# Kernel tuning notes

Measured on AMD Instinct MI355X. Metric: run time of the kernel, lower is better.

## Reference

```python
import jax, jax.numpy as jnp
import numpy as np
from jax.scipy.special import logsumexp

B, N, F_IN, HID = 8, 1024, 256, 128
RATIO = 0.5
NUM_LAYERS = 2
EPS_OT = 0.01  # forward default epsilon


def setup_inputs():
    key = jax.random.key(0)
    ks = jax.random.split(key, 6)
    x = jax.random.normal(ks[0], (B, N, F_IN), dtype=jnp.float32)
    adj = (jax.random.uniform(ks[1], (B, N, N)) < 0.02).astype(jnp.float32)
    adj = jnp.maximum(adj, jnp.swapaxes(adj, 1, 2))  # symmetric sparse-ish graph
    mask = jnp.ones((B, N), dtype=bool)
    W1 = jax.random.normal(ks[2], (F_IN, HID), dtype=jnp.float32) / np.sqrt(F_IN)
    b1 = jnp.zeros((HID,), dtype=jnp.float32)
    Watt = jax.random.normal(ks[3], (HID, 1), dtype=jnp.float32) / np.sqrt(HID)
    batt = jnp.zeros((1,), dtype=jnp.float32)
    W2 = jax.random.normal(ks[4], (HID, F_IN), dtype=jnp.float32) / np.sqrt(HID)
    b2 = jnp.zeros((F_IN,), dtype=jnp.float32)
    return dict(x=x, adj=adj, mask=mask, W1=W1, b1=b1, Watt=Watt, batt=batt,
                W2=W2, b2=b2, opt_epochs=20)


def _gcn_norm(adj):
    # DenseGCNConv add_loop + symmetric normalization
    n = adj.shape[-1]
    A = adj + jnp.eye(n, dtype=adj.dtype)
    d = jnp.maximum(A.sum(-1), 1.0) ** -0.5
    return d[..., :, None] * A * d[..., None, :]


def dense_gcn(x, adj, W, b, mask=None):
    out = jnp.einsum('bij,bjh->bih', _gcn_norm(adj), x @ W) + b
    if mask is not None:
        out = out * mask[..., None].astype(out.dtype)
    return out


def normalize_batch_adj(adj):
    # CoarsenBlock.normalize_batch_adj: self-loop sym-norm, zero-row masked
    n = adj.shape[-1]
    A = adj + jnp.eye(n, dtype=adj.dtype)
    d = jnp.maximum(A.sum(-1), 1.0) ** -0.5
    newA = d[..., :, None] * A * d[..., None, :]
    return (adj.sum(-1) > 0).astype(adj.dtype)[..., None] * newA


def coarsen_block(x, adj, Watt, batt):
    # attention score per node, squared then sigmoid  -> [B, N]
    alpha = jax.nn.sigmoid(dense_gcn(x, adj, Watt, batt) ** 2)[..., 0]
    norm_adj = normalize_batch_adj(adj)
    k = int(adj.shape[1] * RATIO) + 1
    cut = jax.lax.top_k(alpha, k)[0][:, -1]                 # per-sample k-th value
    cut_alpha = jax.nn.relu(alpha + 1e-7 - cut[:, None])    # soft top-k gate
    S = norm_adj * cut_alpha[:, None, :]
    S = S / jnp.maximum(jnp.abs(S).sum(-1, keepdims=True), 1e-12)  # row L1 norm
    emb = jnp.einsum('bij,bif->bjf', S, x)                  # S^T x
    tmp = jnp.einsum('bij,bik->bjk', S, adj)                # S^T adj
    new_adj = jnp.einsum('bjk,bkl->bjl', tmp, S)            # S^T adj S
    return emb, new_adj, S


def sinkhorn_loss(x, y, eps, niter):
    # squared-euclidean cost via gram trick (no [n,m,f] intermediate)
    C = (jnp.sum(x * x, -1)[:, None] + jnp.sum(y * y, -1)[None, :]
         - 2.0 * (x @ y.T))
    n, m = C.shape
    log_mu = jnp.full((n,), -np.log(n), dtype=C.dtype)
    log_nu = jnp.full((m,), -np.log(m), dtype=C.dtype)

    def M(u, v):
        return (-C + u[:, None] + v[None, :]) / eps

    def step(carry, _):
        u, v = carry
        u = eps * (log_mu - logsumexp(M(u, v), axis=1)) + u
        v = eps * (log_nu - logsumexp(M(u, v), axis=0)) + v
        return (u, v), None

    (u, v), _ = jax.lax.scan(step, (jnp.zeros_like(log_mu), jnp.zeros_like(log_nu)),
                             None, length=niter)
    pi = jnp.exp(M(u, v))
    return jnp.sum(pi * C)


def reference(x, adj, mask, W1, b1, Watt, batt, W2, b2, opt_epochs):
    x1 = jax.nn.relu(dense_gcn(x, adj, W1, b1, mask))
    xs0 = x1.mean(axis=1)
    new_adjs = [adj]
    Ss = []
    coarse_x, new_adj = x1, adj
    for _ in range(NUM_LAYERS):
        coarse_x, new_adj, S = coarsen_block(coarse_x, new_adj, Watt, batt)
        new_adjs.append(new_adj)
        Ss.append(S)
    x2 = dense_gcn(coarse_x, new_adj, W2, b2, mask)
    xs1 = x2.mean(axis=1)
    loss_fn = lambda a, b: sinkhorn_loss(a, b, EPS_OT, opt_epochs)
    opt_loss = jnp.sum(jax.vmap(loss_fn)(x, x2))
    return (xs0, xs1, new_adjs[0], new_adjs[1], new_adjs[2], Ss[0], Ss[1], opt_loss)
```

## Files before the change

### kernel.cpp

```cpp
#include <hip/hip_runtime.h>
#include <math.h>

#define BN   8
#define NN   1024
#define FIN  256
#define HIDN 128
#define KTOP 513
#define NITER 20
#define EPS_S 0.01f
#define INV_EPS 100.0f
#define LOG_MU (-6.9314718055994531f)
#define SNB 256

typedef __attribute__((ext_vector_type(8))) short bfrag8;
typedef __attribute__((ext_vector_type(4))) float facc4;

#define GLOAD16(g, l) __builtin_amdgcn_global_load_lds( \
    (const __attribute__((address_space(1))) unsigned int*)(g), \
    (__attribute__((address_space(3))) unsigned int*)(l), 16, 0, 0)

static __device__ __forceinline__ float wred_sum(float s) {
#pragma unroll
  for (int o = 32; o > 0; o >>= 1) s += __shfl_xor(s, o);
  return s;
}
static __device__ __forceinline__ unsigned short f2b(float f) {
  unsigned int u = __float_as_uint(f);
  u += 0x7fff + ((u >> 16) & 1);
  return (unsigned short)(u >> 16);
}
static __device__ __forceinline__ float b2f(unsigned short h) {
  return __uint_as_float((unsigned int)h << 16);
}

template<int WRBF, int WCOPY>
__global__ __launch_bounds__(256) void k_rowstats4(const float* __restrict__ adj,
                                                   float* __restrict__ dv,
                                                   float* __restrict__ rm,
                                                   unsigned short* __restrict__ abf,
                                                   float* __restrict__ ocopy) {
  int r0 = blockIdx.x << 2;
  int t = threadIdx.x, lane = t & 63, wv = t >> 6;
  __shared__ float sm[4][4];
#pragma unroll
  for (int r = 0; r < 4; ++r) {
    float4 v = ((const float4*)(adj + (long)(r0 + r) * NN))[t];
    if (WRBF) {
      ushort4 h; h.x = f2b(v.x); h.y = f2b(v.y); h.z = f2b(v.z); h.w = f2b(v.w);
      *(ushort4*)(abf + (long)(r0 + r) * NN + t * 4) = h;
    }
    if (WCOPY) ((float4*)(ocopy + (long)(r0 + r) * NN))[t] = v;
    float s = (v.x + v.y) + (v.z + v.w);
    s = wred_sum(s);
    if (lane == 0) sm[wv][r] = s;
  }
  __syncthreads();
  if (t < 4) {
    float tot = sm[0][t] + sm[1][t] + sm[2][t] + sm[3][t];
    dv[r0 + t] = rsqrtf(fmaxf(tot + 1.0f, 1.0f));
    rm[r0 + t] = tot > 0.0f ? 1.0f : 0.0f;
  }
}

__global__ __launch_bounds__(256) void k_f2b(const float* __restrict__ X,
                                             unsigned short* __restrict__ Y) {
  long i = ((long)blockIdx.x * 256 + threadIdx.x) * 4;
  float4 v = *(const float4*)(X + i);
  Y[i] = f2b(v.x); Y[i + 1] = f2b(v.y); Y[i + 2] = f2b(v.z); Y[i + 3] = f2b(v.w);
}

__global__ __launch_bounds__(256) void k_w1t(const float* __restrict__ W,
                                             unsigned short* __restrict__ Wt) {
  int idx = blockIdx.x * 256 + threadIdx.x;
  int n = idx >> 8, k = idx & 255;
  Wt[idx] = f2b(W[k * HIDN + n]);
}

__global__ __launch_bounds__(256) void k_prep(const float* __restrict__ X,
                                              unsigned short* __restrict__ Xh,
                                              unsigned short* __restrict__ Xl,
                                              float* __restrict__ sq) {
  int t = threadIdx.x, lane = t & 63, wv = t >> 6;
  int row = blockIdx.x * 4 + wv;
  long base = (long)row * FIN + lane * 4;
  float4 v = *(const float4*)(X + base);
  ushort4 h, l;
  h.x = f2b(v.x); l.x = f2b(v.x - b2f(h.x));
  h.y = f2b(v.y); l.y = f2b(v.y - b2f(h.y));
  h.z = f2b(v.z); l.z = f2b(v.z - b2f(h.z));
  h.w = f2b(v.w); l.w = f2b(v.w - b2f(h.w));
  *(ushort4*)(Xh + base) = h;
  *(ushort4*)(Xl + base) = l;
  float s = v.x * v.x + v.y * v.y + v.z * v.z + v.w * v.w;
  s = wred_sum(s);
  if (lane == 0) sq[row] = s;
}

__global__ __launch_bounds__(256) void k_transp(const float* __restrict__ X,
                                                unsigned short* __restrict__ Xt,
                                                int R, int C) {
  __shared__ float tile[64][65];
  long bb = blockIdx.z;
  const float* Xb = X + bb * (long)R * C;
  unsigned short* Xtb = Xt + bb * (long)R * C;
  int r0 = blockIdx.y * 64, c0 = blockIdx.x * 64;
  int t = threadIdx.x;
  int tr = t >> 4, tc4 = (t & 15) * 4;
#pragma unroll
  for (int p = 0; p < 4; ++p) {
    float4 v = *(const float4*)(Xb + (long)(r0 + tr + p * 16) * C + c0 + tc4);
    tile[tr + p * 16][tc4 + 0] = v.x; tile[tr + p * 16][tc4 + 1] = v.y;
    tile[tr + p * 16][tc4 + 2] = v.z; tile[tr + p * 16][tc4 + 3] = v.w;
  }
  __syncthreads();
  int jj = t >> 2, i0 = (t & 3) * 16;
  unsigned short* orow = Xtb + (long)(c0 + jj) * R + r0 + i0;
#pragma unroll
  for (int q = 0; q < 16; ++q) orow[q] = f2b(tile[i0 + q][jj]);
}

template<int SPLIT>
__global__ __launch_bounds__(256) void k_stc(const float* __restrict__ XW,
                                             const float* __restrict__ dvv,
                                             unsigned short* __restrict__ Bh,
                                             unsigned short* __restrict__ Bl,
                                             int F) {
  __shared__ float tile[64][65];
  __shared__ float dl[64];
  int bz = blockIdx.z;
  const float* Xb = XW + (long)bz * NN * F;
  int j0 = blockIdx.x * 64;
  int n0 = blockIdx.y * 64;
  int t = threadIdx.x;
  int tr = t >> 4, tc4 = (t & 15) * 4;
#pragma unroll
  for (int p = 0; p < 4; ++p) {
    float4 v = *(const float4*)(Xb + (long)(j0 + tr + p * 16) * F + n0 + tc4);
    tile[tr + p * 16][tc4 + 0] = v.x; tile[tr + p * 16][tc4 + 1] = v.y;
    tile[tr + p * 16][tc4 + 2] = v.z; tile[tr + p * 16][tc4 + 3] = v.w;
  }
  if (t < 64) dl[t] = dvv[(bz << 10) + j0 + t];
  __syncthreads();
  int nn = t >> 2, i0 = (t & 3) * 16;
  long obase = ((long)bz * F + n0 + nn) * NN + j0 + i0;
#pragma unroll
  for (int q = 0; q < 16; ++q) {
    float v = tile[i0 + q][nn] * dl[i0 + q];
    unsigned short h = f2b(v);
    Bh[obase + q] = h;
    if (SPLIT) Bl[obase + q] = f2b(v - b2f(h));
  }
}

template<int WF32, int WBF>
__global__ __launch_bounds__(256) void k_mfma_nt(
    const unsigned short* __restrict__ A, const unsigned short* __restrict__ B,
    float* __restrict__ Cf, unsigned short* __restrict__ Cb,
    unsigned short* __restrict__ Cb2,
    int K, int ldA, int ldB, int ldC, long sA, long sB, long sC) {
  __shared__ unsigned short As[128 * 32];
  __shared__ unsigned short Bs[128 * 32];
  int bz = blockIdx.z;
  A += bz * sA; B += bz * sB;
  int m0 = blockIdx.y * 128, n0 = blockIdx.x * 128;
  int tid = threadIdx.x, lane = tid & 63, w = tid >> 6;
  int wr = w >> 1, wc = w & 1;
  facc4 acc[4][4];
#pragma unroll
  for (int i = 0; i < 4; ++i)
#pragma unroll
    for (int j = 0; j < 4; ++j)
#pragma unroll
      for (int q = 0; q < 4; ++q) acc[i][j][q] = 0.f;

  int rA0 = w * 16 + (lane >> 2);
  int kslot = lane & 3;

  for (int k0 = 0; k0 < K; k0 += 32) {
#pragma unroll
    for (int i = 0; i < 2; ++i) {
      int row = i * 64 + rA0;
      int ks = (kslot ^ (row & 3)) << 3;
      GLOAD16(A + (long)(m0 + row) * ldA + k0 + ks, As + (i * 64 + w * 16) * 32);
      GLOAD16(B + (long)(n0 + row) * ldB + k0 + ks, Bs + (i * 64 + w * 16) * 32);
    }
    __syncthreads();
    bfrag8 af[4], bfr[4];
#pragma unroll
    for (int mi = 0; mi < 4; ++mi) {
      int row = wr * 64 + mi * 16 + (lane & 15);
      int sl = (((lane >> 4) ^ (row & 3)) << 3);
      af[mi] = *(const bfrag8*)(As + row * 32 + sl);
    }
#pragma unroll
    for (int ni = 0; ni < 4; ++ni) {
      int row = wc * 64 + ni * 16 + (lane & 15);
      int sl = (((lane >> 4) ^ (row & 3)) << 3);
      bfr[ni] = *(const bfrag8*)(Bs + row * 32 + sl);
    }
#pragma unroll
    for (int mi = 0; mi < 4; ++mi)
#pragma unroll
      for (int ni = 0; ni < 4; ++ni)
        acc[mi][ni] = __builtin_amdgcn_mfma_f32_16x16x32_bf16(
            af[mi], bfr[ni], acc[mi][ni], 0, 0, 0);
    __syncthreads();
  }
  if (WF32) Cf += bz * sC;
  if (WBF) Cb += bz * sC;
  if (WBF == 2) Cb2 += bz * sC;
#pragma unroll
  for (int mi = 0; mi < 4; ++mi) {
    int rowb = m0 + wr * 64 + mi * 16 + ((lane >> 4) << 2);
#pragma unroll
    for (int ni = 0; ni < 4; ++ni) {
      int col = n0 + wc * 64 + ni * 16 + (lane & 15);
#pragma unroll
      for (int q = 0; q < 4; ++q) {
        long off = (long)(rowb + q) * ldC + col;
        float v = acc[mi][ni][q];
        if (WF32) Cf[off] = v;
        if (WBF == 1) Cb[off] = f2b(v);
        if (WBF == 2) {
          unsigned short h = f2b(v);
          Cb[off] = h;
          Cb2[off] = f2b(v - b2f(h));
        }
      }
    }
  }
}

__global__ __launch_bounds__(256) void k_coars(
    const unsigned short* __restrict__ St, const unsigned short* __restrict__ Badj,
    const unsigned short* __restrict__ cxt,
    unsigned short* __restrict__ tmpo, float* __restrict__ embo) {
  __shared__ unsigned short As[128 * 32];
  __shared__ unsigned short Bs[128 * 32];
  int bz = blockIdx.z;
  int bx = blockIdx.x;
  int em = (bx == 8);
  const unsigned short* A = St + (long)bz * 1048576;
  const unsigned short* B = em ? (cxt + (long)bz * 131072)
                               : (Badj + (long)bz * 1048576);
  int m0 = blockIdx.y * 128, n0 = em ? 0 : bx * 128;
  int tid = threadIdx.x, lane = tid & 63, w = tid >> 6;
  int wr = w >> 1, wc = w & 1;
  facc4 acc[4][4];
#pragma unroll
  for (int i = 0; i < 4; ++i)
#pragma unroll
    for (int j = 0; j < 4; ++j)
#pragma unroll
      for (int q = 0; q < 4; ++q) acc[i][j][q] = 0.f;

  int rA0 = w * 16 + (lane >> 2);
  int kslot = lane & 3;

  for (int k0 = 0; k0 < NN; k0 += 32) {
#pragma unroll
    for (int i = 0; i < 2; ++i) {
      int row = i * 64 + rA0;
      int ks = (kslot ^ (row & 3)) << 3;
      GLOAD16(A + (long)(m0 + row) * NN + k0 + ks, As + (i * 64 + w * 16) * 32);
      GLOAD16(B + (long)(n0 + row) * NN + k0 + ks, Bs + (i * 64 + w * 16) * 32);
    }
    __syncthreads();
    bfrag8 af[4], bfr[4];
#pragma unroll
    for (int mi = 0; mi < 4; ++mi) {
      int row = wr * 64 + mi * 16 + (lane & 15);
      int sl = (((lane >> 4) ^ (row & 3)) << 3);
      af[mi] = *(const bfrag8*)(As + row * 32 + sl);
    }
#pragma unroll
    for (int ni = 0; ni < 4; ++ni) {
      int row = wc * 64 + ni * 16 + (lane & 15);
      int sl = (((lane >> 4) ^ (row & 3)) << 3);
      bfr[ni] = *(const bfrag8*)(Bs + row * 32 + sl);
    }
#pragma unroll
    for (int mi = 0; mi < 4; ++mi)
#pragma unroll
      for (int ni = 0; ni < 4; ++ni)
        acc[mi][ni] = __builtin_amdgcn_mfma_f32_16x16x32_bf16(
            af[mi], bfr[ni], acc[mi][ni], 0, 0, 0);
    __syncthreads();
  }
#pragma unroll
  for (int mi = 0; mi < 4; ++mi) {
    int rowb = m0 + wr * 64 + mi * 16 + ((lane >> 4) << 2);
#pragma unroll
    for (int ni = 0; ni < 4; ++ni) {
      int col = n0 + wc * 64 + ni * 16 + (lane & 15);
#pragma unroll
      for (int q = 0; q < 4; ++q) {
        float v = acc[mi][ni][q];
        if (em)
          embo[(long)bz * 131072 + (long)(rowb + q) * HIDN + col] = v;
        else
          tmpo[(long)bz * 1048576 + (long)(rowb + q) * NN + col] = f2b(v);
      }
    }
  }
}

template<int SPLIT, int RELU>
__global__ __launch_bounds__(256) void k_mfma_gcn(
    const unsigned short* __restrict__ Ah, const unsigned short* __restrict__ Al,
    const unsigned short* __restrict__ Bh, const unsigned short* __restrict__ Bl,
    const float* __restrict__ dvv, const float* __restrict__ XW,
    const float* __restrict__ bias, float* __restrict__ Cf, int F) {
  __shared__ unsigned short AsH[128 * 32], BsH[128 * 32];
  __shared__ unsigned short AsL[SPLIT ? 128 * 32 : 16], BsL[SPLIT ? 128 * 32 : 16];
  int bz = blockIdx.z;
  const unsigned short* Ahb = Ah + (long)bz * NN * NN;
  const unsigned short* Alb = SPLIT ? Al + (long)bz * NN * NN : nullptr;
  const unsigned short* Bhb = Bh + (long)bz * F * NN;
  const unsigned short* Blb = SPLIT ? Bl + (long)bz * F * NN : nullptr;
  int m0 = blockIdx.y * 128, n0 = blockIdx.x * 128;
  int tid = threadIdx.x, lane = tid & 63, w = tid >> 6;
  int wr = w >> 1, wc = w & 1;
  facc4 acc[4][4];
#pragma unroll
  for (int i = 0; i < 4; ++i)
#pragma unroll
    for (int j = 0; j < 4; ++j)
#pragma unroll
      for (int q = 0; q < 4; ++q) acc[i][j][q] = 0.f;

  int rA0 = w * 16 + (lane >> 2);
  int kslot = lane & 3;

  for (int k0 = 0; k0 < NN; k0 += 32) {
#pragma unroll
    for (int i = 0; i < 2; ++i) {
      int row = i * 64 + rA0;
      int ks = (kslot ^ (row & 3)) << 3;
      int ld = (i * 64 + w * 16) * 32;
      GLOAD16(Ahb + (long)(m0 + row) * NN + k0 + ks, AsH + ld);
      GLOAD16(Bhb + (long)(n0 + row) * NN + k0 + ks, BsH + ld);
      if (SPLIT) {
        GLOAD16(Alb + (long)(m0 + row) * NN + k0 + ks, AsL + ld);
        GLOAD16(Blb + (long)(n0 + row) * NN + k0 + ks, BsL + ld);
      }
    }
    __syncthreads();
    bfrag8 afh[4], bfh[4], afl[4], bfl[4];
#pragma unroll
    for (int mi = 0; mi < 4; ++mi) {
      int row = wr * 64 + mi * 16 + (lane & 15);
      int sl = (((lane >> 4) ^ (row & 3)) << 3);
      afh[mi] = *(const bfrag8*)(AsH + row * 32 + sl);
      if (SPLIT) afl[mi] = *(const bfrag8*)(AsL + row * 32 + sl);
    }
#pragma unroll
    for (int ni = 0; ni < 4; ++ni) {
      int row = wc * 64 + ni * 16 + (lane & 15);
      int sl = (((lane >> 4) ^ (row & 3)) << 3);
      bfh[ni] = *(const bfrag8*)(BsH + row * 32 + sl);
      if (SPLIT) bfl[ni] = *(const bfrag8*)(BsL + row * 32 + sl);
    }
#pragma unroll
    for (int mi = 0; mi < 4; ++mi)
#pragma unroll
      for (int ni = 0; ni < 4; ++ni) {
        acc[mi][ni] = __builtin_amdgcn_mfma_f32_16x16x32_bf16(
            afh[mi], bfh[ni], acc[mi][ni], 0, 0, 0);
        if (SPLIT) {
          acc[mi][ni] = __builtin_amdgcn_mfma_f32_16x16x32_bf16(
              afh[mi], bfl[ni], acc[mi][ni], 0, 0, 0);
          acc[mi][ni] = __builtin_amdgcn_mfma_f32_16x16x32_bf16(
              afl[mi], bfh[ni], acc[mi][ni], 0, 0, 0);
        }
      }
    __syncthreads();
  }
  Cf += (long)bz * NN * F;
#pragma unroll
  for (int mi = 0; mi < 4; ++mi) {
    int rowb = m0 + wr * 64 + mi * 16 + ((lane >> 4) << 2);
#pragma unroll
    for (int ni = 0; ni < 4; ++ni) {
      int col = n0 + wc * 64 + ni * 16 + (lane & 15);
      float bcol = bias[col];
#pragma unroll
      for (int q = 0; q < 4; ++q) {
        float dm = dvv[(bz << 10) + rowb + q];
        float xwv = XW[((long)(bz << 10) + rowb + q) * F + col];
        float v = dm * (acc[mi][ni][q] + dm * xwv) + bcol;
        if (RELU) v = fmaxf(v, 0.f);
        Cf[(long)(rowb + q) * F + col] = v;
      }
    }
  }
}

__global__ __launch_bounds__(256) void k_mfma_gram(
    const unsigned short* __restrict__ Ah, const unsigned short* __restrict__ Al,
    const unsigned short* __restrict__ Bh, const unsigned short* __restrict__ Bl,
    const float* __restrict__ xx, const float* __restrict__ yy,
    float* __restrict__ Cf, float* __restrict__ Ct) {
  __shared__ unsigned short AsH[128 * 32], AsL[128 * 32];
  __shared__ unsigned short BsH[128 * 32], BsL[128 * 32];
  int bz = blockIdx.z;
  long boff = (long)bz * NN * FIN;
  Ah += boff; Al += boff; Bh += boff; Bl += boff;
  const float* xxb = xx + (bz << 10);
  const float* yyb = yy + (bz << 10);
  int m0 = blockIdx.y * 128, n0 = blockIdx.x * 128;
  int tid = threadIdx.x, lane = tid & 63, w = tid >> 6;
  int wr = w >> 1, wc = w & 1;
  facc4 acc[4][4];
#pragma unroll
  for (int i = 0; i < 4; ++i)
#pragma unroll
    for (int j = 0; j < 4; ++j)
#pragma unroll
      for (int q = 0; q < 4; ++q) acc[i][j][q] = 0.f;

  int rA0 = w * 16 + (lane >> 2);
  int kslot = lane & 3;

  for (int k0 = 0; k0 < FIN; k0 += 32) {
#pragma unroll
    for (int i = 0; i < 2; ++i) {
      int row = i * 64 + rA0;
      int ks = (kslot ^ (row & 3)) << 3;
      long ga = (long)(m0 + row) * FIN + k0 + ks;
      long gb = (long)(n0 + row) * FIN + k0 + ks;
      int ld = (i * 64 + w * 16) * 32;
      GLOAD16(Ah + ga, AsH + ld);
      GLOAD16(Al + ga, AsL + ld);
      GLOAD16(Bh + gb, BsH + ld);
      GLOAD16(Bl + gb, BsL + ld);
    }
    __syncthreads();
    bfrag8 afh[4], afl[4], bfh[4], bfl[4];
#pragma unroll
    for (int mi = 0; mi < 4; ++mi) {
      int row = wr * 64 + mi * 16 + (lane & 15);
      int sl = (((lane >> 4) ^ (row & 3)) << 3);
      afh[mi] = *(const bfrag8*)(AsH + row * 32 + sl);
      afl[mi] = *(const bfrag8*)(AsL + row * 32 + sl);
    }
#pragma unroll
    for (int ni = 0; ni < 4; ++ni) {
      int row = wc * 64 + ni * 16 + (lane & 15);
      int sl = (((lane >> 4) ^ (row & 3)) << 3);
      bfh[ni] = *(const bfrag8*)(BsH + row * 32 + sl);
      bfl[ni] = *(const bfrag8*)(BsL + row * 32 + sl);
    }
#pragma unroll
    for (int mi = 0; mi < 4; ++mi)
#pragma unroll
      for (int ni = 0; ni < 4; ++ni) {
        acc[mi][ni] = __builtin_amdgcn_mfma_f32_16x16x32_bf16(
            afh[mi], bfh[ni], acc[mi][ni], 0, 0, 0);
        acc[mi][ni] = __builtin_amdgcn_mfma_f32_16x16x32_bf16(
            afh[mi], bfl[ni], acc[mi][ni], 0, 0, 0);
        acc[mi][ni] = __builtin_amdgcn_mfma_f32_16x16x32_bf16(
            afl[mi], bfh[ni], acc[mi][ni], 0, 0, 0);
      }
    __syncthreads();
  }
  Cf += (long)bz * NN * NN;
  Ct += (long)bz * NN * NN;
#pragma unroll
  for (int mi = 0; mi < 4; ++mi) {
    int rowb = m0 + wr * 64 + mi * 16 + ((lane >> 4) << 2);
#pragma unroll
    for (int ni = 0; ni < 4; ++ni) {
      int col = n0 + wc * 64 + ni * 16 + (lane & 15);
      float yv = yyb[col];
      float4 tv;
#pragma unroll
      for (int q = 0; q < 4; ++q) {
        float v = xxb[rowb + q] + yv - 2.f * acc[mi][ni][q];
        Cf[(long)(rowb + q) * NN + col] = v;
        ((float*)&tv)[q] = v;
      }
      *(float4*)(Ct + (long)col * NN + rowb) = tv;
    }
  }
}

__global__ __launch_bounds__(256) void k_rowdot(const float* __restrict__ X,
                                                const float* __restrict__ w,
                                                float* __restrict__ out) {
  int t = threadIdx.x; int lane = t & 63; int wv = t >> 6;
  int row = blockIdx.x * 4 + wv;
  const float* xr = X + (long)row * HIDN;
  float s = xr[lane] * w[lane] + xr[lane + 64] * w[lane + 64];
  s = wred_sum(s);
  if (lane == 0) out[row] = s;
}

__global__ __launch_bounds__(256) void k_alpha4(const float* __restrict__ adj,
                                                const float* __restrict__ dv,
                                                const float* __restrict__ s0,
                                                const float* __restrict__ batt,
                                                float* __restrict__ alpha) {
  int r0 = blockIdx.x << 2; int b = r0 >> 10; int i0 = r0 & (NN - 1);
  int t = threadIdx.x, lane = t & 63, wv = t >> 6;
  float4 d4 = ((const float4*)(dv + (b << 10)))[t];
  float4 s4 = ((const float4*)(s0 + (b << 10)))[t];
  float w4[4];
  w4[0] = d4.x * s4.x; w4[1] = d4.y * s4.y; w4[2] = d4.z * s4.z; w4[3] = d4.w * s4.w;
  __shared__ float sm[4][4];
#pragma unroll
  for (int r = 0; r < 4; ++r) {
    float4 a4 = ((const float4*)(adj + (long)(r0 + r) * NN))[t];
    float dot = a4.x * w4[0] + a4.y * w4[1] + a4.z * w4[2] + a4.w * w4[3];
    int i = i0 + r;
    if ((i >> 2) == t) dot += w4[i & 3];
    dot = wred_sum(dot);
    if (lane == 0) sm[wv][r] = dot;
  }
  __syncthreads();
  if (t < 4) {
    float dot = sm[0][t] + sm[1][t] + sm[2][t] + sm[3][t];
    float tt = dv[r0 + t] * dot + batt[0];
    alpha[r0 + t] = 1.f / (1.f + __expf(-tt * tt));
  }
}

__global__ __launch_bounds__(512) void k_topk(const float* __restrict__ alpha,
                                              float* __restrict__ cut) {
  __shared__ float smv[NN];
  int b = blockIdx.x; int t = threadIdx.x;
  smv[t] = alpha[(b << 10) + t];
  smv[t + 512] = alpha[(b << 10) + t + 512];
  __syncthreads();
  for (int k2 = 2; k2 <= NN; k2 <<= 1) {
    for (int j2 = k2 >> 1; j2 > 0; j2 >>= 1) {
      int i = ((t / j2) * (j2 << 1)) + (t % j2);
      int ixj = i + j2;
      bool up = ((i & k2) == 0);
      float a = smv[i], c = smv[ixj];
      if ((a > c) == up) { smv[i] = c; smv[ixj] = a; }
      __syncthreads();
    }
  }
  if (t == 0) cut[b] = smv[NN - KTOP];
}

__global__ __launch_bounds__(256) void k_sbuild4(const float* __restrict__ adj,
                                                 const float* __restrict__ dv,
                                                 const float* __restrict__ rm,
                                                 const float* __restrict__ alpha,
                                                 const float* __restrict__ cut,
                                                 float* __restrict__ S) {
  int r0 = blockIdx.x << 2; int b = r0 >> 10; int i0 = r0 & (NN - 1);
  int t = threadIdx.x, lane = t & 63, wv = t >> 6;
  float cb = cut[b];
  float4 d4 = ((const float4*)(dv + (b << 10)))[t];
  float4 al4 = ((const float4*)(alpha + (b << 10)))[t];
  float4 dg;
  dg.x = d4.x * fmaxf(al4.x + 1e-7f - cb, 0.f);
  dg.y = d4.y * fmaxf(al4.y + 1e-7f - cb, 0.f);
  dg.z = d4.z * fmaxf(al4.z + 1e-7f - cb, 0.f);
  dg.w = d4.w * fmaxf(al4.w + 1e-7f - cb, 0.f);
  __shared__ float sm[4][4];
  __shared__ float sinv[4];
  float4 vals[4];
#pragma unroll
  for (int r = 0; r < 4; ++r) {
    float di = dv[r0 + r] * rm[r0 + r];
    float4 a4 = ((const float4*)(adj + (long)(r0 + r) * NN))[t];
    int i = i0 + r;
    if ((i >> 2) == t) ((float*)&a4)[i & 3] += 1.f;
    vals[r].x = di * dg.x * a4.x; vals[r].y = di * dg.y * a4.y;
    vals[r].z = di * dg.z * a4.z; vals[r].w = di * dg.w * a4.w;
    float s = (fabsf(vals[r].x) + fabsf(vals[r].y)) +
              (fabsf(vals[r].z) + fabsf(vals[r].w));
    s = wred_sum(s);
    if (lane == 0) sm[wv][r] = s;
  }
  __syncthreads();
  if (t < 4) sinv[t] = 1.f / fmaxf(sm[0][t] + sm[1][t] + sm[2][t] + sm[3][t], 1e-12f);
  __syncthreads();
#pragma unroll
  for (int r = 0; r < 4; ++r) {
    float inv = sinv[r];
    float4 o; o.x = vals[r].x * inv; o.y = vals[r].y * inv;
    o.z = vals[r].z * inv; o.w = vals[r].w * inv;
    ((float4*)(S + (long)(r0 + r) * NN))[t] = o;
  }
}

template<int GCN>
__global__ __launch_bounds__(256) void k_gemm_ks(
    const float* __restrict__ A, const float* __restrict__ Bm, float* __restrict__ P,
    int M, int Nn, int K, int KS, long sA, long sB,
    const float* __restrict__ dv) {
  __shared__ float As[8][132];
  __shared__ float Bs[8][132];
  int z = blockIdx.z;
  int b = z / KS, ks = z % KS;
  int KC = K / KS;
  A += (long)b * sA; Bm += (long)b * sB;
  const float* dvb = GCN ? (dv + (long)b * NN) : nullptr;
  int m0 = blockIdx.y * 128, n0 = blockIdx.x * 128;
  int tid = threadIdx.x;
  int tx = tid & 15, ty = tid >> 4;
  float acc[8][8];
#pragma unroll
  for (int i = 0; i < 8; i++)
#pragma unroll
    for (int j = 0; j < 8; j++) acc[i][j] = 0.f;

  float drow = 0.f;
  if (GCN) drow = dvb[m0 + (tid >> 1)];

  for (int k0 = ks * KC; k0 < ks * KC + KC; k0 += 8) {
    {
      int r = tid >> 1, c4 = (tid & 1) * 4;
      float4 av = *(const float4*)(A + (long)(m0 + r) * K + k0 + c4);
      float a4[4] = {av.x, av.y, av.z, av.w};
      if (GCN) {
#pragma unroll
        for (int q = 0; q < 4; ++q) {
          int gj = k0 + c4 + q;
          float val = a4[q] + ((m0 + r) == gj ? 1.f : 0.f);
          a4[q] = drow * dvb[gj] * val;
        }
      }
      As[c4 + 0][r] = a4[0]; As[c4 + 1][r] = a4[1];
      As[c4 + 2][r] = a4[2]; As[c4 + 3][r] = a4[3];
    }
    {
      int kr = tid >> 5, c4 = (tid & 31) * 4;
      float4 bv = *(const float4*)(Bm + (long)(k0 + kr) * Nn + n0 + c4);
      *(float4*)&Bs[kr][c4] = bv;
    }
    __syncthreads();
#pragma unroll
    for (int k = 0; k < 8; ++k) {
      float av[8], bv[8];
      *(float4*)&av[0] = *(const float4*)&As[k][ty * 8];
      *(float4*)&av[4] = *(const float4*)&As[k][ty * 8 + 4];
      *(float4*)&bv[0] = *(const float4*)&Bs[k][tx * 8];
      *(float4*)&bv[4] = *(const float4*)&Bs[k][tx * 8 + 4];
#pragma unroll
      for (int i = 0; i < 8; i++)
#pragma unroll
        for (int j = 0; j < 8; j++)
          acc[i][j] = fmaf(av[i], bv[j], acc[i][j]);
    }
    __syncthreads();
  }
  float* Pz = P + (long)z * M * Nn;
#pragma unroll
  for (int i = 0; i < 8; ++i) {
    int m = m0 + ty * 8 + i;
    float* prow = Pz + (long)m * Nn + n0 + tx * 8;
    *(float4*)&prow[0] = *(float4*)&acc[i][0];
    *(float4*)&prow[4] = *(float4*)&acc[i][4];
  }
}

template<int RELU, int BIAS>
__global__ __launch_bounds__(256) void k_red_bias(
    const float* __restrict__ P, const float* __restrict__ bias,
    float* __restrict__ out, int Nn, int KS, long chunk) {
  long u = ((long)blockIdx.x * 256 + threadIdx.x) * 4;
  long b = u / chunk; long rem = u % chunk;
  const float* p = P + b * KS * chunk + rem;
  float4 s = *(const float4*)p;
  for (int k = 1; k < KS; ++k) {
    float4 q = *(const float4*)(p + (long)k * chunk);
    s.x += q.x; s.y += q.y; s.z += q.z; s.w += q.w;
  }
  if (BIAS) {
    int n = (int)(rem % Nn);
    s.x += bias[n]; s.y += bias[n + 1]; s.z += bias[n + 2]; s.w += bias[n + 3];
  }
  if (RELU) {
    s.x = fmaxf(s.x, 0.f); s.y = fmaxf(s.y, 0.f);
    s.z = fmaxf(s.z, 0.f); s.w = fmaxf(s.w, 0.f);
  }
  *(float4*)(out + u) = s;
}

__global__ __launch_bounds__(256) void k_colmean(const float* __restrict__ X, int Fd,
                                                 float* __restrict__ out) {
  int nb = Fd >> 6;
  int b = blockIdx.x / nb; int f0 = (blockIdx.x % nb) << 6;
  int t = threadIdx.x;
  int f = f0 + (t & 63); int rc = t >> 6;
  const float* xb = X + (long)b * NN * Fd;
  float s = 0.f;
  for (int i = rc * 256; i < rc * 256 + 256; ++i) s += xb[(long)i * Fd + f];
  __shared__ float sm[256];
  sm[t] = s; __syncthreads();
  if (t < 64) out[b * Fd + f] = (sm[t] + sm[t + 64] + sm[t + 128] + sm[t + 192]) * (1.f / NN);
}


static __device__ __forceinline__ float4 load_cohere4(const float* p) {
  float4 v;
  asm volatile("global_load_dwordx4 %0, %1, off sc0 sc1\n\ts_waitcnt vmcnt(0)"
               : "=v"(v) : "v"(p) : "memory");
  return v;
}
static __device__ __forceinline__ float load_cohere1(const float* p) {
  float v;
  asm volatile("global_load_dword %0, %1, off sc0 sc1\n\ts_waitcnt vmcnt(0)"
               : "=v"(v) : "v"(p) : "memory");
  return v;
}
static __device__ __forceinline__ void store_cohere1(float* p, float v) {
  asm volatile("global_store_dword %0, %1, off sc0 sc1\n\ts_waitcnt vmcnt(0)"
               :: "v"(p), "v"(v) : "memory");
}

static __device__ __forceinline__ void stage_vec(float* __restrict__ vls,
                                                 const float* __restrict__ src,
                                                 int t) {
  if (t < 256) {
    float4 v = load_cohere4(src + t * 4);
    *(float4*)(vls + t * 4) = v;
  }
  __syncthreads();
}

static __device__ __forceinline__ void group_bar(int* __restrict__ slots,
                                                 int bid, int grp, int t, int g1) {
  __syncthreads();
  if (t == 0)
    __hip_atomic_store(&slots[bid * 16], g1, __ATOMIC_RELAXED,
                       __HIP_MEMORY_SCOPE_AGENT);
  if (t < 32) {
    int idx = ((t << 3) + grp) * 16;
    int spin = 0;
    while (__hip_atomic_load(&slots[idx], __ATOMIC_RELAXED,
                             __HIP_MEMORY_SCOPE_AGENT) < g1) {
      if (++spin > (1 << 20)) break;
      __builtin_amdgcn_s_sleep(1);
    }
  }
  __syncthreads();
}

template<int LOSS>
static __device__ __forceinline__ void pass_reg(const float4 (&Cr)[16],
    const float* __restrict__ vls, float* __restrict__ uout,
    int jc, int row, float* __restrict__ lossacc) {
  float4 vr[16];
#pragma unroll
  for (int k = 0; k < 16; ++k)
    vr[k] = *(const float4*)(vls + (k * 16 + jc) * 4);
  float mx = -3.0e38f;
#pragma unroll
  for (int k = 0; k < 16; ++k) {
    float ax = vr[k].x - Cr[k].x, ay = vr[k].y - Cr[k].y;
    float az = vr[k].z - Cr[k].z, aw = vr[k].w - Cr[k].w;
    mx = fmaxf(mx, fmaxf(fmaxf(ax, ay), fmaxf(az, aw)));
  }
#pragma unroll
  for (int m = 1; m <= 8; m <<= 1) mx = fmaxf(mx, __shfl_xor(mx, m));
  float ls = 0.f, ld = 0.f;
#pragma unroll
  for (int k = 0; k < 16; ++k) {
    float e;
    e = __expf(vr[k].x - Cr[k].x - mx); ls += e; if (LOSS) ld = fmaf(e, Cr[k].x, ld);
    e = __expf(vr[k].y - Cr[k].y - mx); ls += e; if (LOSS) ld = fmaf(e, Cr[k].y, ld);
    e = __expf(vr[k].z - Cr[k].z - mx); ls += e; if (LOSS) ld = fmaf(e, Cr[k].z, ld);
    e = __expf(vr[k].w - Cr[k].w - mx); ls += e; if (LOSS) ld = fmaf(e, Cr[k].w, ld);
  }
#pragma unroll
  for (int m = 1; m <= 8; m <<= 1) {
    ls += __shfl_xor(ls, m);
    if (LOSS) ld += __shfl_xor(ld, m);
  }
  if (jc == 0) {
    float uval = LOG_MU - (mx + __logf(ls));
    store_cohere1(uout + row, uval);
    if (LOSS) *lossacc += (ld / ls) * (1.0f / 1024.0f);
  }
}

__global__ __launch_bounds__(512, 2) void k_sink_reg(
    const float* __restrict__ Cm, const float* __restrict__ Ct,
    float* __restrict__ uvv, float* __restrict__ vvv,
    float* __restrict__ part, float* __restrict__ oloss,
    int* __restrict__ slots1, int* __restrict__ slots2) {
  int bid = blockIdx.x, t = threadIdx.x, lane = t & 63, wvi = t >> 6;
  int jc = lane & 15;
  int grp = bid & 7;
  int inner = bid >> 3;
  int row = (grp << 10) + inner * 32 + wvi * 4 + (lane >> 4);
  __shared__ float vls[1024];
  float4 Creg[16], Ctreg[16];
  {
    const float4* cp = (const float4*)(Cm + (long)row * NN);
    const float4* tp = (const float4*)(Ct + (long)row * NN);
#pragma unroll
    for (int k = 0; k < 16; ++k) {
      float4 c = cp[k * 16 + jc], ct = tp[k * 16 + jc];
      Creg[k].x = c.x * INV_EPS;  Creg[k].y = c.y * INV_EPS;
      Creg[k].z = c.z * INV_EPS;  Creg[k].w = c.w * INV_EPS;
      Ctreg[k].x = ct.x * INV_EPS; Ctreg[k].y = ct.y * INV_EPS;
      Ctreg[k].z = ct.z * INV_EPS; Ctreg[k].w = ct.w * INV_EPS;
    }
  }
  const float* ub = uvv + (grp << 10);
  const float* vb = vvv + (grp << 10);
  float lossacc = 0.f;
  int g1 = 1;
  for (int it = 0; it < NITER; ++it) {
    stage_vec(vls, vb, t);
    pass_reg<0>(Creg, vls, uvv, jc, row, nullptr);
    group_bar(slots1, bid, grp, t, g1); ++g1;
    stage_vec(vls, ub, t);
    if (it < NITER - 1) {
      pass_reg<0>(Ctreg, vls, vvv, jc, row, nullptr);
      group_bar(slots1, bid, grp, t, g1); ++g1;
    } else {
      pass_reg<1>(Ctreg, vls, vvv, jc, row, &lossacc);
    }
  }
  float s = wred_sum(lossacc);
  __shared__ float lsm[8];
  if (lane == 0) lsm[wvi] = s;
  __syncthreads();
  if (t == 0) {
    float ps = 0.f;
#pragma unroll
    for (int i = 0; i < 8; ++i) ps += lsm[i];
    store_cohere1(part + bid, ps);
    __hip_atomic_store(&slots2[bid * 16], 1, __ATOMIC_RELAXED,
                       __HIP_MEMORY_SCOPE_AGENT);
  }
  if (bid == 0) {
    if (t < SNB) {
      int spin = 0;
      while (__hip_atomic_load(&slots2[t * 16], __ATOMIC_RELAXED,
                               __HIP_MEMORY_SCOPE_AGENT) < 1) {
        if (++spin > (1 << 20)) break;
        __builtin_amdgcn_s_sleep(1);
      }
    }
    __syncthreads();
    float s2 = 0.f;
    if (t < SNB) s2 = load_cohere1(part + t);
    s2 = wred_sum(s2);
    __shared__ float sm2[8];
    if (lane == 0) sm2[wvi] = s2;
    __syncthreads();
    if (t == 0) {
      float tot = 0.f;
#pragma unroll
      for (int i = 0; i < 8; ++i) tot += sm2[i];
      oloss[0] = tot * EPS_S;
    }
  }
}

extern "C" void kernel_launch(void* const* d_in, const int* in_sizes, int n_in,
                              void* d_out, int out_size, void* d_ws, size_t ws_size,
                              hipStream_t stream) {
  const float* x    = (const float*)d_in[0];
  const float* adj  = (const float*)d_in[1];
  const float* W1   = (const float*)d_in[3];
  const float* b1   = (const float*)d_in[4];
  const float* Watt = (const float*)d_in[5];
  const float* batt = (const float*)d_in[6];
  const float* W2   = (const float*)d_in[7];
  const float* b2   = (const float*)d_in[8];

  float* out = (float*)d_out;
  float* xs0   = out;
  float* xs1   = out + 1024;
  float* oadj0 = out + 3072;
  float* oadj1 = oadj0 + 8388608;
  float* oadj2 = oadj1 + 8388608;
  float* oS0   = oadj2 + 8388608;
  float* oS1   = oS0 + 8388608;
  float* oloss = oS1 + 8388608;

  float* ws   = (float*)d_ws;
  float* wXW  = ws;
  float* wCXA = wXW + 2097152;
  float* wCXB = wCXA + 1048576;
  float* wR   = wCXB + 1048576;
  float* wX2  = wR + 8388608;
  float* wStf = wX2 + 2097152;
  float* wCxtf= wStf + 4194304;
  float* wCt  = wCxtf + 524288;
  float* smb  = wCt + 8388608;

  unsigned short* tmp_bf = (unsigned short*)wR;
  unsigned short* a2h    = (unsigned short*)wCt;
  unsigned short* a2l    = a2h + 8388608;
  unsigned short* adj_bf = (unsigned short*)oadj2;
  unsigned short* St     = (unsigned short*)wStf;
  unsigned short* cxt    = (unsigned short*)wCxtf;
  unsigned short* x_bf   = (unsigned short*)wStf;
  unsigned short* Bg1    = (unsigned short*)wCxtf;
  unsigned short* Bg2h   = (unsigned short*)wStf;
  unsigned short* Bg2l   = (unsigned short*)(wStf + 2097152);
  unsigned short* xh  = (unsigned short*)wStf;
  unsigned short* xl  = xh + 2097152;
  unsigned short* x2h = xh + 4194304;
  unsigned short* x2l = xh + 6291456;
  float* Cmat = wR;
  float* d0 = smb;            float* rm0 = smb + 8192;
  float* d1 = smb + 16384;    float* rm1 = smb + 24576;
  float* d2 = smb + 32768;    float* rm2 = smb + 40960;
  float* s0v = smb + 49152;   float* alp = smb + 57344;
  float* xxv = smb + 65536;   float* yyv = smb + 73728;
  float* uv  = smb + 81920;   float* vv  = smb + 90112;
  float* cutv = smb + 98304;  float* part = smb + 98368;
  unsigned short* W1t = (unsigned short*)(smb + 98624);
  int* ibar = (int*)(smb + 115008);
  int* slots1 = ibar;
  int* slots2 = ibar + 4096;

  k_rowstats4<1, 1><<<2048, 256, 0, stream>>>(adj, d0, rm0, adj_bf, oadj0);

  k_f2b<<<2048, 256, 0, stream>>>(x, x_bf);
  k_w1t<<<128, 256, 0, stream>>>(W1, W1t);
  k_mfma_nt<1, 0><<<dim3(1, 64, 1), 256, 0, stream>>>(x_bf, W1t, wXW, nullptr,
      nullptr, 256, 256, 256, 128, 0L, 0L, 0L);
  k_stc<0><<<dim3(16, 2, 8), 256, 0, stream>>>(wXW, d0, Bg1, nullptr, HIDN);
  k_mfma_gcn<0, 1><<<dim3(1, 8, 8), 256, 0, stream>>>(adj_bf, nullptr, Bg1,
      nullptr, d0, wXW, b1, wCXA, HIDN);
  k_colmean<<<16, 256, 0, stream>>>(wCXA, HIDN, xs0);

  k_rowdot<<<2048, 256, 0, stream>>>(wCXA, Watt, s0v);
  k_alpha4<<<2048, 256, 0, stream>>>(adj, d0, s0v, batt, alp);
  k_topk<<<8, 512, 0, stream>>>(alp, cutv);
  k_sbuild4<<<2048, 256, 0, stream>>>(adj, d0, rm0, alp, cutv, oS0);
  k_transp<<<dim3(16, 16, 8), 256, 0, stream>>>(oS0, St, 1024, 1024);
  k_transp<<<dim3(2, 16, 8), 256, 0, stream>>>(wCXA, cxt, 1024, 128);
  k_coars<<<dim3(9, 8, 8), 256, 0, stream>>>(St, adj_bf, cxt, tmp_bf, wCXB);
  k_mfma_nt<1, 1><<<dim3(8, 8, 8), 256, 0, stream>>>(tmp_bf, St, oadj1, adj_bf,
      nullptr, 1024, 1024, 1024, 1024, 1048576L, 1048576L, 1048576L);
  k_rowstats4<0, 0><<<2048, 256, 0, stream>>>(oadj1, d1, rm1, nullptr, nullptr);

  k_rowdot<<<2048, 256, 0, stream>>>(wCXB, Watt, s0v);
  k_alpha4<<<2048, 256, 0, stream>>>(oadj1, d1, s0v, batt, alp);
  k_topk<<<8, 512, 0, stream>>>(alp, cutv);
  k_sbuild4<<<2048, 256, 0, stream>>>(oadj1, d1, rm1, alp, cutv, oS1);
  k_transp<<<dim3(16, 16, 8), 256, 0, stream>>>(oS1, St, 1024, 1024);
  k_transp<<<dim3(2, 16, 8), 256, 0, stream>>>(wCXB, cxt, 1024, 128);
  k_coars<<<dim3(9, 8, 8), 256, 0, stream>>>(St, adj_bf, cxt, tmp_bf, wCXA);
  k_mfma_nt<1, 2><<<dim3(8, 8, 8), 256, 0, stream>>>(tmp_bf, St, oadj2, a2h,
      a2l, 1024, 1024, 1024, 1024, 1048576L, 1048576L, 1048576L);
  k_rowstats4<0, 0><<<2048, 256, 0, stream>>>(oadj2, d2, rm2, nullptr, nullptr);

  k_gemm_ks<0><<<dim3(2, 64, 2), 256, 0, stream>>>(wCXA, W2, wR, 8192, FIN, HIDN,
      2, 0L, 0L, nullptr);
  k_red_bias<0, 0><<<2048, 256, 0, stream>>>(wR, nullptr, wXW, FIN, 2, 2097152L);
  k_stc<1><<<dim3(16, 4, 8), 256, 0, stream>>>(wXW, d2, Bg2h, Bg2l, FIN);
  k_mfma_gcn<1, 0><<<dim3(2, 8, 8), 256, 0, stream>>>(a2h, a2l, Bg2h, Bg2l,
      d2, wXW, b2, wX2, FIN);
  k_colmean<<<32, 256, 0, stream>>>(wX2, FIN, xs1);

  k_prep<<<2048, 256, 0, stream>>>(x, xh, xl, xxv);
  k_prep<<<2048, 256, 0, stream>>>(wX2, x2h, x2l, yyv);
  k_mfma_gram<<<dim3(8, 8, 8), 256, 0, stream>>>(xh, xl, x2h, x2l, xxv, yyv,
      Cmat, wCt);
  hipMemsetAsync(uv, 0, (size_t)2 * 8192 * 4, stream);
  hipMemsetAsync(ibar, 0, (size_t)8192 * 4, stream);
  k_sink_reg<<<SNB, 512, 0, stream>>>(Cmat, wCt, uv, vv, part, oloss,
                                      slots1, slots2);
}
```

Baseline: 743.3 us.

## Replace Sinkhorn group barriers with sentinel-polled multi-buffered dual vectors

The persistent Sinkhorn kernel no longer uses an explicit group barrier with slot counters. Each half-iteration now writes its dual vector into a fresh buffer that was pre-filled with a 0xFFFFFFFF sentinel, and consumers spin on the data itself until the sentinel is gone. This removes one synchronization round-trip per half-step. The logsumexp also reuses the previous max, recomputing it only if the sum falls out of range, and splits its reductions into four accumulators. The two prep launches are merged into one. This costs 41 buffers of memsets up front and relies on the sentinel never appearing as a real value.

```diff
diff --git a/kernel.cpp b/kernel.cpp
--- a/kernel.cpp
+++ b/kernel.cpp
@@ -11,6 +11,7 @@
 #define INV_EPS 100.0f
 #define LOG_MU (-6.9314718055994531f)
 #define SNB 256
+#define SENTU 0xFFFFFFFFu
 
 typedef __attribute__((ext_vector_type(8))) short bfrag8;
 typedef __attribute__((ext_vector_type(4))) float facc4;
@@ -76,12 +77,17 @@
   Wt[idx] = f2b(W[k * HIDN + n]);
 }
 
-__global__ __launch_bounds__(256) void k_prep(const float* __restrict__ X,
-                                              unsigned short* __restrict__ Xh,
-                                              unsigned short* __restrict__ Xl,
-                                              float* __restrict__ sq) {
+__global__ __launch_bounds__(256) void k_prep2(
+    const float* __restrict__ X0, const float* __restrict__ X1,
+    unsigned short* __restrict__ Xh0, unsigned short* __restrict__ Xl0,
+    unsigned short* __restrict__ Xh1, unsigned short* __restrict__ Xl1,
+    float* __restrict__ sq0, float* __restrict__ sq1) {
+  int bb = blockIdx.x;
+  const float* X; unsigned short* Xh; unsigned short* Xl; float* sq; int rb;
+  if (bb < 2048) { X = X0; Xh = Xh0; Xl = Xl0; sq = sq0; rb = bb; }
+  else { X = X1; Xh = Xh1; Xl = Xl1; sq = sq1; rb = bb - 2048; }
   int t = threadIdx.x, lane = t & 63, wv = t >> 6;
-  int row = blockIdx.x * 4 + wv;
+  int row = rb * 4 + wv;
   long base = (long)row * FIN + lane * 4;
   float4 v = *(const float4*)(X + base);
   ushort4 h, l;
@@ -698,9 +704,9 @@
 }
 
 
-static __device__ __forceinline__ float4 load_cohere4(const float* p) {
-  float4 v;
-  asm volatile("global_load_dwordx4 %0, %1, off sc0 sc1\n\ts_waitcnt vmcnt(0)"
+static __device__ __forceinline__ float2 load_cohere2(const float* p) {
+  float2 v;
+  asm volatile("global_load_dwordx2 %0, %1, off sc0 sc1\n\ts_waitcnt vmcnt(0)"
                : "=v"(v) : "v"(p) : "memory");
   return v;
 }
@@ -715,77 +721,110 @@
                :: "v"(p), "v"(v) : "memory");
 }
 
-static __device__ __forceinline__ void stage_vec(float* __restrict__ vls,
-                                                 const float* __restrict__ src,
-                                                 int t) {
-  if (t < 256) {
-    float4 v = load_cohere4(src + t * 4);
-    *(float4*)(vls + t * 4) = v;
+static __device__ __forceinline__ void pollstage(const float* __restrict__ src,
+                                                 float* __restrict__ vls, int t) {
+  float2 v; int spin = 0;
+  for (;;) {
+    v = load_cohere2(src + t * 2);
+    if ((__float_as_uint(v.x) != SENTU) & (__float_as_uint(v.y) != SENTU)) break;
+    if (++spin > (1 << 20)) break;
+    __builtin_amdgcn_s_sleep(1);
   }
   __syncthreads();
-}
-
-static __device__ __forceinline__ void group_bar(int* __restrict__ slots,
-                                                 int bid, int grp, int t, int g1) {
+  *(float2*)(vls + t * 2) = v;
   __syncthreads();
-  if (t == 0)
-    __hip_atomic_store(&slots[bid * 16], g1, __ATOMIC_RELAXED,
-                       __HIP_MEMORY_SCOPE_AGENT);
-  if (t < 32) {
-    int idx = ((t << 3) + grp) * 16;
-    int spin = 0;
-    while (__hip_atomic_load(&slots[idx], __ATOMIC_RELAXED,
-                             __HIP_MEMORY_SCOPE_AGENT) < g1) {
-      if (++spin > (1 << 20)) break;
-      __builtin_amdgcn_s_sleep(1);
-    }
-  }
-  __syncthreads();
-}
-
-template<int LOSS>
+}
+
+template<int LOSS, int STORE>
 static __device__ __forceinline__ void pass_reg(const float4 (&Cr)[16],
-    const float* __restrict__ vls, float* __restrict__ uout,
-    int jc, int row, float* __restrict__ lossacc) {
+    const float* __restrict__ vls, float* __restrict__ dbout,
+    int jc, int row, float* __restrict__ lossacc, float& mxs, int fresh) {
   float4 vr[16];
 #pragma unroll
   for (int k = 0; k < 16; ++k)
     vr[k] = *(const float4*)(vls + (k * 16 + jc) * 4);
-  float mx = -3.0e38f;
-#pragma unroll
-  for (int k = 0; k < 16; ++k) {
-    float ax = vr[k].x - Cr[k].x, ay = vr[k].y - Cr[k].y;
-    float az = vr[k].z - Cr[k].z, aw = vr[k].w - Cr[k].w;
-    mx = fmaxf(mx, fmaxf(fmaxf(ax, ay), fmaxf(az, aw)));
-  }
-#pragma unroll
-  for (int m = 1; m <= 8; m <<= 1) mx = fmaxf(mx, __shfl_xor(mx, m));
-  float ls = 0.f, ld = 0.f;
-#pragma unroll
-  for (int k = 0; k < 16; ++k) {
-    float e;
-    e = __expf(vr[k].x - Cr[k].x - mx); ls += e; if (LOSS) ld = fmaf(e, Cr[k].x, ld);
-    e = __expf(vr[k].y - Cr[k].y - mx); ls += e; if (LOSS) ld = fmaf(e, Cr[k].y, ld);
-    e = __expf(vr[k].z - Cr[k].z - mx); ls += e; if (LOSS) ld = fmaf(e, Cr[k].z, ld);
-    e = __expf(vr[k].w - Cr[k].w - mx); ls += e; if (LOSS) ld = fmaf(e, Cr[k].w, ld);
+  float mx = mxs;
+  if (fresh) {
+    float m0 = -3.0e38f, m1 = m0, m2 = m0, m3 = m0;
+#pragma unroll
+    for (int k = 0; k < 16; ++k) {
+      m0 = fmaxf(m0, vr[k].x - Cr[k].x);
+      m1 = fmaxf(m1, vr[k].y - Cr[k].y);
+      m2 = fmaxf(m2, vr[k].z - Cr[k].z);
+      m3 = fmaxf(m3, vr[k].w - Cr[k].w);
+    }
+    mx = fmaxf(fmaxf(m0, m1), fmaxf(m2, m3));
+#pragma unroll
+    for (int m = 1; m <= 8; m <<= 1) mx = fmaxf(mx, __shfl_xor(mx, m));
+  }
+  float ls, ld = 0.f;
+  {
+    float s0 = 0, s1 = 0, s2 = 0, s3 = 0, d0 = 0, d1 = 0, d2 = 0, d3 = 0;
+#pragma unroll
+    for (int k = 0; k < 16; ++k) {
+      float e0 = __expf(vr[k].x - Cr[k].x - mx);
+      float e1 = __expf(vr[k].y - Cr[k].y - mx);
+      float e2 = __expf(vr[k].z - Cr[k].z - mx);
+      float e3 = __expf(vr[k].w - Cr[k].w - mx);
+      s0 += e0; s1 += e1; s2 += e2; s3 += e3;
+      if (LOSS) {
+        d0 = fmaf(e0, Cr[k].x, d0); d1 = fmaf(e1, Cr[k].y, d1);
+        d2 = fmaf(e2, Cr[k].z, d2); d3 = fmaf(e3, Cr[k].w, d3);
+      }
+    }
+    ls = (s0 + s1) + (s2 + s3);
+    if (LOSS) ld = (d0 + d1) + (d2 + d3);
   }
 #pragma unroll
   for (int m = 1; m <= 8; m <<= 1) {
     ls += __shfl_xor(ls, m);
     if (LOSS) ld += __shfl_xor(ld, m);
   }
+  if (!(ls > 1e-25f && ls < 1e25f)) {
+    float m0 = -3.0e38f, m1 = m0, m2 = m0, m3 = m0;
+#pragma unroll
+    for (int k = 0; k < 16; ++k) {
+      m0 = fmaxf(m0, vr[k].x - Cr[k].x);
+      m1 = fmaxf(m1, vr[k].y - Cr[k].y);
+      m2 = fmaxf(m2, vr[k].z - Cr[k].z);
+      m3 = fmaxf(m3, vr[k].w - Cr[k].w);
+    }
+    mx = fmaxf(fmaxf(m0, m1), fmaxf(m2, m3));
+#pragma unroll
+    for (int m = 1; m <= 8; m <<= 1) mx = fmaxf(mx, __shfl_xor(mx, m));
+    float s0 = 0, s1 = 0, s2 = 0, s3 = 0, d0 = 0, d1 = 0, d2 = 0, d3 = 0;
+#pragma unroll
+    for (int k = 0; k < 16; ++k) {
+      float e0 = __expf(vr[k].x - Cr[k].x - mx);
+      float e1 = __expf(vr[k].y - Cr[k].y - mx);
+      float e2 = __expf(vr[k].z - Cr[k].z - mx);
+      float e3 = __expf(vr[k].w - Cr[k].w - mx);
+      s0 += e0; s1 += e1; s2 += e2; s3 += e3;
+      if (LOSS) {
+        d0 = fmaf(e0, Cr[k].x, d0); d1 = fmaf(e1, Cr[k].y, d1);
+        d2 = fmaf(e2, Cr[k].z, d2); d3 = fmaf(e3, Cr[k].w, d3);
+      }
+    }
+    ls = (s0 + s1) + (s2 + s3);
+    if (LOSS) ld = (d0 + d1) + (d2 + d3);
+#pragma unroll
+    for (int m = 1; m <= 8; m <<= 1) {
+      ls += __shfl_xor(ls, m);
+      if (LOSS) ld += __shfl_xor(ld, m);
+    }
+  }
+  mxs = mx;
   if (jc == 0) {
     float uval = LOG_MU - (mx + __logf(ls));
-    store_cohere1(uout + row, uval);
+    if (STORE) store_cohere1(dbout + row, uval);
     if (LOSS) *lossacc += (ld / ls) * (1.0f / 1024.0f);
   }
 }
 
-__global__ __launch_bounds__(512, 2) void k_sink_reg(
+__global__ __launch_bounds__(512, 1) void k_sink_reg(
     const float* __restrict__ Cm, const float* __restrict__ Ct,
-    float* __restrict__ uvv, float* __restrict__ vvv,
-    float* __restrict__ part, float* __restrict__ oloss,
-    int* __restrict__ slots1, int* __restrict__ slots2) {
+    float* __restrict__ db, float* __restrict__ part,
+    float* __restrict__ oloss) {
   int bid = blockIdx.x, t = threadIdx.x, lane = t & 63, wvi = t >> 6;
   int jc = lane & 15;
   int grp = bid & 7;
@@ -805,20 +844,24 @@
       Ctreg[k].z = ct.z * INV_EPS; Ctreg[k].w = ct.w * INV_EPS;
     }
   }
-  const float* ub = uvv + (grp << 10);
-  const float* vb = vvv + (grp << 10);
+  {
+    float2 v = *(const float2*)(db + (grp << 10) + t * 2);
+    *(float2*)(vls + t * 2) = v;
+  }
+  __syncthreads();
   float lossacc = 0.f;
-  int g1 = 1;
+  float mxu = 0.f, mxv = 0.f;
+  int g = 1;
   for (int it = 0; it < NITER; ++it) {
-    stage_vec(vls, vb, t);
-    pass_reg<0>(Creg, vls, uvv, jc, row, nullptr);
-    group_bar(slots1, bid, grp, t, g1); ++g1;
-    stage_vec(vls, ub, t);
+    pass_reg<0, 1>(Creg, vls, db + (long)g * 8192, jc, row, nullptr, mxu, it == 0);
+    pollstage(db + (long)g * 8192 + (grp << 10), vls, t);
+    ++g;
     if (it < NITER - 1) {
-      pass_reg<0>(Ctreg, vls, vvv, jc, row, nullptr);
-      group_bar(slots1, bid, grp, t, g1); ++g1;
+      pass_reg<0, 1>(Ctreg, vls, db + (long)g * 8192, jc, row, nullptr, mxv, it == 0);
+      pollstage(db + (long)g * 8192 + (grp << 10), vls, t);
+      ++g;
     } else {
-      pass_reg<1>(Ctreg, vls, vvv, jc, row, &lossacc);
+      pass_reg<1, 0>(Ctreg, vls, nullptr, jc, row, &lossacc, mxv, 0);
     }
   }
   float s = wred_sum(lossacc);
@@ -830,21 +873,18 @@
 #pragma unroll
     for (int i = 0; i < 8; ++i) ps += lsm[i];
     store_cohere1(part + bid, ps);
-    __hip_atomic_store(&slots2[bid * 16], 1, __ATOMIC_RELAXED,
-                       __HIP_MEMORY_SCOPE_AGENT);
   }
   if (bid == 0) {
+    float s2 = 0.f;
     if (t < SNB) {
       int spin = 0;
-      while (__hip_atomic_load(&slots2[t * 16], __ATOMIC_RELAXED,
-                               __HIP_MEMORY_SCOPE_AGENT) < 1) {
-        if (++spin > (1 << 20)) break;
+      for (;;) {
+        s2 = load_cohere1(part + t);
+        if (__float_as_uint(s2) != SENTU) break;
+        if (++spin > (1 << 20)) { s2 = 0.f; break; }
         __builtin_amdgcn_s_sleep(1);
       }
     }
-    __syncthreads();
-    float s2 = 0.f;
-    if (t < SNB) s2 = load_cohere1(part + t);
     s2 = wred_sum(s2);
     __shared__ float sm2[8];
     if (lane == 0) sm2[wvi] = s2;
@@ -911,12 +951,13 @@
   float* d2 = smb + 32768;    float* rm2 = smb + 40960;
   float* s0v = smb + 49152;   float* alp = smb + 57344;
   float* xxv = smb + 65536;   float* yyv = smb + 73728;
-  float* uv  = smb + 81920;   float* vv  = smb + 90112;
   float* cutv = smb + 98304;  float* part = smb + 98368;
   unsigned short* W1t = (unsigned short*)(smb + 98624);
-  int* ibar = (int*)(smb + 115008);
-  int* slots1 = ibar;
-  int* slots2 = ibar + 4096;
+  float* db = smb + 131072;
+
+  hipMemsetAsync(db, 0, (size_t)8192 * 4, stream);
+  hipMemsetAsync(db + 8192, 0xFF, (size_t)40 * 8192 * 4, stream);
+  hipMemsetAsync(part, 0xFF, (size_t)256 * 4, stream);
 
   k_rowstats4<1, 1><<<2048, 256, 0, stream>>>(adj, d0, rm0, adj_bf, oadj0);
 
@@ -959,12 +1000,8 @@
       d2, wXW, b2, wX2, FIN);
   k_colmean<<<32, 256, 0, stream>>>(wX2, FIN, xs1);
 
-  k_prep<<<2048, 256, 0, stream>>>(x, xh, xl, xxv);
-  k_prep<<<2048, 256, 0, stream>>>(wX2, x2h, x2l, yyv);
+  k_prep2<<<4096, 256, 0, stream>>>(x, wX2, xh, xl, x2h, x2l, xxv, yyv);
   k_mfma_gram<<<dim3(8, 8, 8), 256, 0, stream>>>(xh, xl, x2h, x2l, xxv, yyv,
       Cmat, wCt);
-  hipMemsetAsync(uv, 0, (size_t)2 * 8192 * 4, stream);
-  hipMemsetAsync(ibar, 0, (size_t)8192 * 4, stream);
-  k_sink_reg<<<SNB, 512, 0, stream>>>(Cmat, wCt, uv, vv, part, oloss,
-                                      slots1, slots2);
-}
+  k_sink_reg<<<SNB, 512, 0, stream>>>(Cmat, wCt, db, part, oloss);
+}
```

After: 752.8 us. About the same (+1.3%).
